# Performance work log

Measured on AMD Instinct MI355X. Metric: run time of the kernel, lower is better.

Reference implementation:

```python
import jax, jax.numpy as jnp
import numpy as np

N, E, G = 50000, 1250000, 256
IN, H, OUT = 64, 64, 2


def _glorot(k, shape):
    fan = shape[0] + shape[1]
    return jax.random.normal(k, shape, jnp.float32) * np.float32(np.sqrt(2.0 / fan))


def setup_inputs() -> dict:
    key = jax.random.key(0)
    ks = jax.random.split(key, 24)
    inp = {
        "x": jax.random.normal(ks[0], (N, IN), jnp.float32),
        "edge_index": jax.random.randint(ks[1], (2, E), 0, N, dtype=jnp.int32),
        "edge_weight": jax.random.uniform(ks[2], (E,), jnp.float32),
        "batch": jnp.sort(jax.random.randint(ks[3], (N,), 0, G, dtype=jnp.int32)),
    }
    # TransformerConv layer 1 (in=IN -> out=H, heads=1, edge_dim=1)
    inp["Wq1"] = _glorot(ks[4], (IN, H)); inp["bq1"] = jnp.zeros((H,), jnp.float32)
    inp["Wk1"] = _glorot(ks[5], (IN, H)); inp["bk1"] = jnp.zeros((H,), jnp.float32)
    inp["Wv1"] = _glorot(ks[6], (IN, H)); inp["bv1"] = jnp.zeros((H,), jnp.float32)
    inp["We1"] = _glorot(ks[7], (1, H))
    inp["Ws1"] = _glorot(ks[8], (IN, H)); inp["bs1"] = jnp.zeros((H,), jnp.float32)
    # TransformerConv layer 2 (H -> H)
    inp["Wq2"] = _glorot(ks[9], (H, H)); inp["bq2"] = jnp.zeros((H,), jnp.float32)
    inp["Wk2"] = _glorot(ks[10], (H, H)); inp["bk2"] = jnp.zeros((H,), jnp.float32)
    inp["Wv2"] = _glorot(ks[11], (H, H)); inp["bv2"] = jnp.zeros((H,), jnp.float32)
    inp["We2"] = _glorot(ks[12], (1, H))
    inp["Ws2"] = _glorot(ks[13], (H, H)); inp["bs2"] = jnp.zeros((H,), jnp.float32)
    # final linear
    inp["Wl"] = _glorot(ks[14], (H, OUT)); inp["bl"] = jnp.zeros((OUT,), jnp.float32)
    return inp


def _tconv(x, src, dst, e_attr, Wq, bq, Wk, bk, Wv, bv, We, Ws, bs, n):
    # PyG TransformerConv, heads=1, concat=True, root_weight=True, beta=False.
    d = Wq.shape[1]
    q = (x @ Wq + bq)[dst]            # [E, d] gather at target nodes
    k = (x @ Wk + bk)[src]            # [E, d] gather at source nodes
    v = (x @ Wv + bv)[src]            # [E, d]
    e = e_attr @ We                   # [E, d] edge embedding (no bias in PyG)
    alpha = jnp.sum(q * (k + e), axis=-1) / jnp.sqrt(jnp.float32(d))  # [E]
    # segment softmax over incoming edges of each target node
    amax = jax.ops.segment_max(alpha, dst, num_segments=n)
    amax = jnp.where(jnp.isfinite(amax), amax, jnp.float32(0.0))
    ex = jnp.exp(alpha - amax[dst])
    denom = jax.ops.segment_sum(ex, dst, num_segments=n)
    w = ex / jnp.maximum(denom[dst], jnp.float32(1e-16))
    out = jax.ops.segment_sum(w[:, None] * (v + e), dst, num_segments=n)  # [n, d]
    return out + x @ Ws + bs          # skip connection (lin_skip)


def reference(x, edge_index, edge_weight, batch,
              Wq1, bq1, Wk1, bk1, Wv1, bv1, We1, Ws1, bs1,
              Wq2, bq2, Wk2, bk2, Wv2, bv2, We2, Ws2, bs2,
              Wl, bl):
    src, dst = edge_index[0], edge_index[1]
    ea = edge_weight[:, None]  # edge_weight.unsqueeze(-1), edge_dim=1
    n = x.shape[0]
    h = jax.nn.relu(_tconv(x, src, dst, ea, Wq1, bq1, Wk1, bk1, Wv1, bv1, We1, Ws1, bs1, n))
    h = jax.nn.relu(_tconv(h, src, dst, ea, Wq2, bq2, Wk2, bk2, Wv2, bv2, We2, Ws2, bs2, n))
    # global_mean_pool over batch ids
    cnt = jax.ops.segment_sum(jnp.ones((n,), jnp.float32), batch, num_segments=G)
    pooled = jax.ops.segment_sum(h, batch, num_segments=G) / jnp.maximum(cnt, 1.0)[:, None]
    return pooled @ Wl + bl
```

## Files before the change

### kernel.cpp

```cpp
#include <hip/hip_runtime.h>
#include <hip/hip_fp16.h>

#define NN 50000
#define NE 1250000
#define NE4 312500
#define NG 256
#define NBKT 782
#define BCAP 2048
#define TILE 4096
#define NTB 306

#define QSCALE 0.18033688011112042f
#define EXP2 __builtin_amdgcn_exp2f

#if defined(__has_builtin)
#  if __has_builtin(__builtin_amdgcn_fdot2)
#    define HAS_FDOT2 1
#  endif
#endif

typedef _Float16 h2vec __attribute__((ext_vector_type(2)));

static __device__ __forceinline__ float fdot2f(unsigned a, unsigned b, float c) {
#ifdef HAS_FDOT2
    return __builtin_amdgcn_fdot2(__builtin_bit_cast(h2vec, a),
                                  __builtin_bit_cast(h2vec, b), c, false);
#else
    float2 fa = __half22float2(__builtin_bit_cast(__half2, a));
    float2 fb = __half22float2(__builtin_bit_cast(__half2, b));
    return fmaf(fa.x, fb.x, fmaf(fa.y, fb.y, c));
#endif
}

static __device__ __forceinline__ unsigned h2u(__half2 h) {
    return __builtin_bit_cast(unsigned, h);
}

__global__ void k_zero(int* __restrict__ gCursor) {
    int i = blockIdx.x * 256 + threadIdx.x;
    if (i < NBKT) gCursor[i] = 0;
}

__global__ void k_bscatter(const int* __restrict__ src, const int* __restrict__ dst,
                           const float* __restrict__ ew, int* __restrict__ gCursor,
                           unsigned* __restrict__ bbuf) {
    __shared__ int cnt[NBKT];
    __shared__ int base[NBKT];
    for (int i = threadIdx.x; i < NBKT; i += 256) cnt[i] = 0;
    __syncthreads();
    const int4* s4 = (const int4*)src;
    const int4* d4 = (const int4*)dst;
    const float4* w4 = (const float4*)ew;
    int b4 = blockIdx.x * (TILE / 4);
    unsigned rec[16]; int bkt[16];
    #pragma unroll
    for (int j = 0; j < 4; j++) {
        int i4 = b4 + j * 256 + threadIdx.x;
        if (i4 < NE4) {
            int4 s = s4[i4]; int4 d = d4[i4]; float4 w = w4[i4];
            int b0 = d.x >> 6, b1 = d.y >> 6, b2 = d.z >> 6, b3 = d.w >> 6;
            bkt[4*j+0] = b0; bkt[4*j+1] = b1; bkt[4*j+2] = b2; bkt[4*j+3] = b3;
            rec[4*j+0] = (unsigned)s.x | ((unsigned)(d.x & 63) << 16) | ((unsigned)(w.x * 1023.f + 0.5f) << 22);
            rec[4*j+1] = (unsigned)s.y | ((unsigned)(d.y & 63) << 16) | ((unsigned)(w.y * 1023.f + 0.5f) << 22);
            rec[4*j+2] = (unsigned)s.z | ((unsigned)(d.z & 63) << 16) | ((unsigned)(w.z * 1023.f + 0.5f) << 22);
            rec[4*j+3] = (unsigned)s.w | ((unsigned)(d.w & 63) << 16) | ((unsigned)(w.w * 1023.f + 0.5f) << 22);
            atomicAdd(&cnt[b0], 1); atomicAdd(&cnt[b1], 1);
            atomicAdd(&cnt[b2], 1); atomicAdd(&cnt[b3], 1);
        } else {
            bkt[4*j+0] = -1; bkt[4*j+1] = -1; bkt[4*j+2] = -1; bkt[4*j+3] = -1;
        }
    }
    __syncthreads();
    for (int i = threadIdx.x; i < NBKT; i += 256)
        base[i] = cnt[i] ? (i << 11) + atomicAdd(&gCursor[i], cnt[i]) : 0;
    __syncthreads();
    #pragma unroll
    for (int j = 0; j < 16; j++) {
        if (bkt[j] >= 0) {
            int pos = atomicAdd(&base[bkt[j]], 1);
            if (pos < ((bkt[j] + 1) << 11)) bbuf[pos] = rec[j];
        }
    }
}

__global__ void k_bsort(const int* __restrict__ gCursor, const unsigned* __restrict__ bbuf,
                        int* __restrict__ off, int* __restrict__ deg,
                        unsigned* __restrict__ pairP) {
    int b = blockIdx.x;
    int st = b << 11;
    int ce = gCursor[b]; if (ce > BCAP) ce = BCAP;
    __shared__ unsigned sbuf[BCAP];
    __shared__ int h[64];
    __shared__ int cur[64];
    if (threadIdx.x < 64) h[threadIdx.x] = 0;
    __syncthreads();
    for (int i = threadIdx.x; i < ce; i += 256) {
        unsigned r = bbuf[st + i];
        sbuf[i] = r;
        atomicAdd(&h[(r >> 16) & 63], 1);
    }
    __syncthreads();
    if (threadIdx.x < 64) {
        int v = h[threadIdx.x];
        int inc = v;
        #pragma unroll
        for (int o = 1; o < 64; o <<= 1) {
            int tmp = __shfl_up(inc, o);
            if (threadIdx.x >= o) inc += tmp;
        }
        int exc = st + inc - v;
        cur[threadIdx.x] = exc;
        int n = b * 64 + threadIdx.x;
        if (n < NN) { off[n] = exc; deg[n] = v; }
    }
    __syncthreads();
    for (int i = threadIdx.x; i < ce; i += 256) {
        unsigned r = sbuf[i];
        int pos = atomicAdd(&cur[(r >> 16) & 63], 1);
        float w = (float)(r >> 22) * (1.f / 1023.f);
        unsigned hw = (unsigned)__half_as_ushort(__float2half(w));
        pairP[pos] = (r & 0xFFFFu) | (hw << 16);
    }
}

__global__ __launch_bounds__(256, 4)
void k_linear(const float* __restrict__ xin,
              const float* __restrict__ Wq, const float* __restrict__ bq,
              const float* __restrict__ Wk, const float* __restrict__ bk,
              const float* __restrict__ Wv, const float* __restrict__ bv,
              const float* __restrict__ Ws, const float* __restrict__ bs,
              __half* __restrict__ qh, __half* __restrict__ kvh,
              float* __restrict__ agg) {
    int tid = threadIdx.x;
    int mat = tid >> 6, feat = tid & 63;
    const float* W = mat == 0 ? Wq : mat == 1 ? Wk : mat == 2 ? Wv : Ws;
    const float* b = mat == 0 ? bq : mat == 1 ? bk : mat == 2 ? bv : bs;

    float wcol[64];
    #pragma unroll
    for (int k = 0; k < 64; k++) wcol[k] = W[k * 64 + feat];
    float bias = b[feat];
    int kvoff = feat + (mat == 2 ? 64 : 0);

    __shared__ __align__(16) float sx[16 * 64];
    const float4* x4 = (const float4*)xin;

    int n0 = blockIdx.x * 16;
    if (n0 >= NN) return;
    float4 nxt = x4[n0 * 16 + tid];
    int stride = gridDim.x * 16;

    for (; n0 < NN; n0 += stride) {
        __syncthreads();
        ((float4*)sx)[tid] = nxt;
        __syncthreads();
        int n1 = n0 + stride;
        if (n1 < NN) nxt = x4[n1 * 16 + tid];
        for (int c = 0; c < 16; c++) {
            const float4* sxc = (const float4*)(sx + c * 64);
            float a0 = bias, a1 = 0.f, a2 = 0.f, a3 = 0.f;
            #pragma unroll
            for (int k4 = 0; k4 < 16; k4 += 4) {
                float4 v0 = sxc[k4 + 0], v1 = sxc[k4 + 1];
                float4 v2 = sxc[k4 + 2], v3 = sxc[k4 + 3];
                a0 = fmaf(v0.x, wcol[4 * k4 + 0], a0);
                a0 = fmaf(v0.y, wcol[4 * k4 + 1], a0);
                a0 = fmaf(v0.z, wcol[4 * k4 + 2], a0);
                a0 = fmaf(v0.w, wcol[4 * k4 + 3], a0);
                a1 = fmaf(v1.x, wcol[4 * k4 + 4], a1);
                a1 = fmaf(v1.y, wcol[4 * k4 + 5], a1);
                a1 = fmaf(v1.z, wcol[4 * k4 + 6], a1);
                a1 = fmaf(v1.w, wcol[4 * k4 + 7], a1);
                a2 = fmaf(v2.x, wcol[4 * k4 + 8], a2);
                a2 = fmaf(v2.y, wcol[4 * k4 + 9], a2);
                a2 = fmaf(v2.z, wcol[4 * k4 + 10], a2);
                a2 = fmaf(v2.w, wcol[4 * k4 + 11], a2);
                a3 = fmaf(v3.x, wcol[4 * k4 + 12], a3);
                a3 = fmaf(v3.y, wcol[4 * k4 + 13], a3);
                a3 = fmaf(v3.z, wcol[4 * k4 + 14], a3);
                a3 = fmaf(v3.w, wcol[4 * k4 + 15], a3);
            }
            float acc = (a0 + a1) + (a2 + a3);
            int nn = n0 + c;
            if (mat == 0)      qh[nn * 64 + feat] = __float2half(acc * QSCALE);
            else if (mat == 3) agg[nn * 64 + feat] = acc;
            else               kvh[nn * 128 + kvoff] = __float2half(acc);
        }
    }
}

__global__ void k_edge(const unsigned* __restrict__ pairP, const int* __restrict__ off,
                       const int* __restrict__ deg,
                       const __half* __restrict__ qh, const uint4* __restrict__ kv16,
                       const float* __restrict__ We, const float* __restrict__ aggin,
                       float* __restrict__ outp) {
    long gid = (long)blockIdx.x * 256 + threadIdx.x;
    int n = (int)(gid >> 6);
    if (n >= NN) return;
    int lane = threadIdx.x & 63;
    int g = lane >> 3, l = lane & 7;

    const uint4* q4 = (const uint4*)qh;
    uint4 qu = q4[n * 8 + l];
    const float4* wp = (const float4*)(We + l * 8);
    float4 wa = wp[0], wb = wp[1];
    unsigned we01 = h2u(__floats2half2_rn(wa.x, wa.y));
    unsigned we23 = h2u(__floats2half2_rn(wa.z, wa.w));
    unsigned we45 = h2u(__floats2half2_rn(wb.x, wb.y));
    unsigned we67 = h2u(__floats2half2_rn(wb.z, wb.w));

    int st = off[n], dg = deg[n];

    float qwe = fdot2f(qu.x, we01, fdot2f(qu.y, we23,
                fdot2f(qu.z, we45, fdot2f(qu.w, we67, 0.f))));
    qwe += __shfl_xor(qwe, 1); qwe += __shfl_xor(qwe, 2); qwe += __shfl_xor(qwe, 4);

    float den = 0.f, sw = 0.f;
    float acc[8] = {0.f, 0.f, 0.f, 0.f, 0.f, 0.f, 0.f, 0.f};

    auto edge = [&](unsigned pr, uint4 kk, uint4 vv) {
        float w = __half2float(__ushort_as_half((unsigned short)(pr >> 16)));
        float tA = fdot2f(qu.x, kk.x, fdot2f(qu.y, kk.y, 0.f));
        float tB = fdot2f(qu.z, kk.z, fdot2f(qu.w, kk.w, 0.f));
        float t = tA + tB;
        t += __shfl_xor(t, 1); t += __shfl_xor(t, 2); t += __shfl_xor(t, 4);
        t = fmaf(w, qwe, t);
        float p = EXP2(t);
        den += p;
        sw = fmaf(p, w, sw);
        float2 v0 = __half22float2(__builtin_bit_cast(__half2, vv.x));
        float2 v1 = __half22float2(__builtin_bit_cast(__half2, vv.y));
        float2 v2 = __half22float2(__builtin_bit_cast(__half2, vv.z));
        float2 v3 = __half22float2(__builtin_bit_cast(__half2, vv.w));
        acc[0] = fmaf(p, v0.x, acc[0]); acc[1] = fmaf(p, v0.y, acc[1]);
        acc[2] = fmaf(p, v1.x, acc[2]); acc[3] = fmaf(p, v1.y, acc[3]);
        acc[4] = fmaf(p, v2.x, acc[4]); acc[5] = fmaf(p, v2.y, acc[5]);
        acc[6] = fmaf(p, v3.x, acc[6]); acc[7] = fmaf(p, v3.y, acc[7]);
    };

    int nfull = dg >> 3;
    if (nfull > 0) {
        unsigned prA = pairP[st + g];
        unsigned prB = (nfull > 1) ? pairP[st + 8 + g] : 0u;
        unsigned rowA = prA & 0xFFFFu;
        uint4 kkA = kv16[rowA * 16 + l];
        uint4 vvA = kv16[rowA * 16 + 8 + l];
        for (int i = 0; i + 1 < nfull; i++) {
            unsigned prC = (i + 2 < nfull) ? pairP[st + (i + 2) * 8 + g] : 0u;
            unsigned rowB = prB & 0xFFFFu;
            uint4 kkB = kv16[rowB * 16 + l];
            uint4 vvB = kv16[rowB * 16 + 8 + l];
            edge(prA, kkA, vvA);
            prA = prB; kkA = kkB; vvA = vvB; prB = prC;
        }
        edge(prA, kkA, vvA);
    }
    int tl = nfull * 8 + g;
    if (tl < dg) {
        unsigned pr = pairP[st + tl];
        unsigned row = pr & 0xFFFFu;
        uint4 kk = kv16[row * 16 + l];
        uint4 vv = kv16[row * 16 + 8 + l];
        edge(pr, kk, vv);
    }

    #pragma unroll
    for (int o = 8; o <= 32; o <<= 1) {
        den += __shfl_xor(den, o);
        sw  += __shfl_xor(sw, o);
        #pragma unroll
        for (int j = 0; j < 8; j++) acc[j] += __shfl_xor(acc[j], o);
    }

    if (g == 0) {
        float inv = 1.f / fmaxf(den, 1e-16f);
        float swi = sw * inv;
        const float4* ain = (const float4*)(aggin + n * 64 + l * 8);
        float4 a0 = ain[0], a1 = ain[1];
        a0.x = fmaxf(fmaf(acc[0], inv, fmaf(swi, wa.x, a0.x)), 0.f);
        a0.y = fmaxf(fmaf(acc[1], inv, fmaf(swi, wa.y, a0.y)), 0.f);
        a0.z = fmaxf(fmaf(acc[2], inv, fmaf(swi, wa.z, a0.z)), 0.f);
        a0.w = fmaxf(fmaf(acc[3], inv, fmaf(swi, wa.w, a0.w)), 0.f);
        a1.x = fmaxf(fmaf(acc[4], inv, fmaf(swi, wb.x, a1.x)), 0.f);
        a1.y = fmaxf(fmaf(acc[5], inv, fmaf(swi, wb.y, a1.y)), 0.f);
        a1.z = fmaxf(fmaf(acc[6], inv, fmaf(swi, wb.z, a1.z)), 0.f);
        a1.w = fmaxf(fmaf(acc[7], inv, fmaf(swi, wb.w, a1.w)), 0.f);
        float4* ao = (float4*)(outp + n * 64 + l * 8);
        ao[0] = a0; ao[1] = a1;
    }
}

__global__ void k_final(const float* __restrict__ h, const int* __restrict__ batch,
                        const float* __restrict__ Wl, const float* __restrict__ bl,
                        float* __restrict__ out) {
    int g = blockIdx.x;
    int tid = threadIdx.x;
    int lo = 0, hi = NN;
    while (lo < hi) { int mid = (lo + hi) >> 1; if (batch[mid] < g) lo = mid + 1; else hi = mid; }
    int s0 = lo;
    hi = NN;
    while (lo < hi) { int mid = (lo + hi) >> 1; if (batch[mid] < g + 1) lo = mid + 1; else hi = mid; }
    int s1 = lo;

    int sub = tid >> 6, lane = tid & 63;
    float a = 0.f;
    for (int n = s0 + sub; n < s1; n += 4) a += h[n * 64 + lane];
    __shared__ float sred[4][64];
    sred[sub][lane] = a;
    __syncthreads();
    if (tid < 64) {
        float p = (sred[0][tid] + sred[1][tid] + sred[2][tid] + sred[3][tid])
                  / fmaxf((float)(s1 - s0), 1.f);
        float a0 = p * Wl[tid * 2 + 0];
        float a1 = p * Wl[tid * 2 + 1];
        #pragma unroll
        for (int o = 1; o < 64; o <<= 1) { a0 += __shfl_xor(a0, o); a1 += __shfl_xor(a1, o); }
        if (tid == 0) { out[g * 2 + 0] = a0 + bl[0]; out[g * 2 + 1] = a1 + bl[1]; }
    }
}

extern "C" void kernel_launch(void* const* d_in, const int* in_sizes, int n_in,
                              void* d_out, int out_size, void* d_ws, size_t ws_size,
                              hipStream_t stream) {
    const float* x    = (const float*)d_in[0];
    const int*   ei   = (const int*)d_in[1];
    const float* ew   = (const float*)d_in[2];
    const int*   batch= (const int*)d_in[3];
    const float *Wq1 = (const float*)d_in[4],  *bq1 = (const float*)d_in[5],
                *Wk1 = (const float*)d_in[6],  *bk1 = (const float*)d_in[7],
                *Wv1 = (const float*)d_in[8],  *bv1 = (const float*)d_in[9],
                *We1 = (const float*)d_in[10], *Ws1 = (const float*)d_in[11],
                *bs1 = (const float*)d_in[12],
                *Wq2 = (const float*)d_in[13], *bq2 = (const float*)d_in[14],
                *Wk2 = (const float*)d_in[15], *bk2 = (const float*)d_in[16],
                *Wv2 = (const float*)d_in[17], *bv2 = (const float*)d_in[18],
                *We2 = (const float*)d_in[19], *Ws2 = (const float*)d_in[20],
                *bs2 = (const float*)d_in[21],
                *Wl  = (const float*)d_in[22], *bl  = (const float*)d_in[23];
    const int* src = ei;
    const int* dst = ei + NE;
    float* out = (float*)d_out;

    float* p = (float*)d_ws;
    float* agg1 = p; p += (size_t)NN * 64;
    float* agg2 = p; p += (size_t)NN * 64;
    __half* qh  = (__half*)p; p += (size_t)NN * 32;
    __half* kvh = (__half*)p; p += (size_t)NN * 64;
    unsigned* bbuf  = (unsigned*)p; p += (size_t)NBKT * BCAP;
    unsigned* pairP = (unsigned*)p; p += (size_t)NBKT * BCAP;
    int* gCursor = (int*)p; p += NBKT;
    int* off     = (int*)p; p += NN;
    int* deg     = (int*)p; p += NN;

    dim3 b256(256);
    int wgrid = (int)(((long)NN * 64 + 255) / 256);

    k_zero<<<4, b256, 0, stream>>>(gCursor);
    k_bscatter<<<NTB, b256, 0, stream>>>(src, dst, ew, gCursor, bbuf);
    k_bsort<<<NBKT, b256, 0, stream>>>(gCursor, bbuf, off, deg, pairP);

    k_linear<<<1024, b256, 0, stream>>>(x, Wq1, bq1, Wk1, bk1, Wv1, bv1, Ws1, bs1,
                                        qh, kvh, agg1);
    k_edge<<<wgrid, b256, 0, stream>>>(pairP, off, deg, qh, (const uint4*)kvh, We1,
                                       agg1, agg1);

    k_linear<<<1024, b256, 0, stream>>>(agg1, Wq2, bq2, Wk2, bk2, Wv2, bv2, Ws2, bs2,
                                        qh, kvh, agg2);
    k_edge<<<wgrid, b256, 0, stream>>>(pairP, off, deg, qh, (const uint4*)kvh, We2,
                                       agg2, agg2);

    k_final<<<NG, b256, 0, stream>>>(agg2, batch, Wl, bl, out);
}
```

Baseline: 207.8 us.

## Stage bucket scatter and per-node sort in LDS for coalesced global writes

Measured after the change: 219.6 us. 5.7% more time.

```diff
diff --git a/kernel.cpp b/kernel.cpp
--- a/kernel.cpp
+++ b/kernel.cpp
@@ -45,7 +45,11 @@
                            const float* __restrict__ ew, int* __restrict__ gCursor,
                            unsigned* __restrict__ bbuf) {
     __shared__ int cnt[NBKT];
-    __shared__ int base[NBKT];
+    __shared__ int gbase[NBKT];
+    __shared__ int spos[NBKT];
+    __shared__ int sscan[256];
+    __shared__ unsigned staged[TILE];
+    __shared__ unsigned short sbkt[TILE];
     for (int i = threadIdx.x; i < NBKT; i += 256) cnt[i] = 0;
     __syncthreads();
     const int4* s4 = (const int4*)src;
@@ -71,15 +75,47 @@
         }
     }
     __syncthreads();
-    for (int i = threadIdx.x; i < NBKT; i += 256)
-        base[i] = cnt[i] ? (i << 11) + atomicAdd(&gCursor[i], cnt[i]) : 0;
+    int t = threadIdx.x;
+    int c[4]; int sum = 0;
+    #pragma unroll
+    for (int j = 0; j < 4; j++) {
+        int b = t * 4 + j;
+        c[j] = (b < NBKT) ? cnt[b] : 0;
+        sum += c[j];
+    }
+    sscan[t] = sum;
+    __syncthreads();
+    for (int o = 1; o < 256; o <<= 1) {
+        int tmp = (t >= o) ? sscan[t - o] : 0;
+        __syncthreads();
+        sscan[t] += tmp;
+        __syncthreads();
+    }
+    int run = sscan[t] - sum;
+    #pragma unroll
+    for (int j = 0; j < 4; j++) {
+        int b = t * 4 + j;
+        if (b < NBKT) {
+            spos[b] = run;
+            if (c[j]) gbase[b] = (b << 11) + atomicAdd(&gCursor[b], c[j]);
+            run += c[j];
+        }
+    }
     __syncthreads();
     #pragma unroll
     for (int j = 0; j < 16; j++) {
         if (bkt[j] >= 0) {
-            int pos = atomicAdd(&base[bkt[j]], 1);
-            if (pos < ((bkt[j] + 1) << 11)) bbuf[pos] = rec[j];
-        }
+            int p = atomicAdd(&spos[bkt[j]], 1);
+            staged[p] = rec[j];
+            sbkt[p] = (unsigned short)bkt[j];
+        }
+    }
+    __syncthreads();
+    int total = sscan[255];
+    for (int i = threadIdx.x; i < total; i += 256) {
+        int b = sbkt[i];
+        int gdest = gbase[b] + (i - (spos[b] - cnt[b]));
+        if (gdest < ((b + 1) << 11)) bbuf[gdest] = staged[i];
     }
 }
 
@@ -90,6 +126,7 @@
     int st = b << 11;
     int ce = gCursor[b]; if (ce > BCAP) ce = BCAP;
     __shared__ unsigned sbuf[BCAP];
+    __shared__ unsigned sout[BCAP];
     __shared__ int h[64];
     __shared__ int cur[64];
     if (threadIdx.x < 64) h[threadIdx.x] = 0;
@@ -108,10 +145,10 @@
             int tmp = __shfl_up(inc, o);
             if (threadIdx.x >= o) inc += tmp;
         }
-        int exc = st + inc - v;
+        int exc = inc - v;
         cur[threadIdx.x] = exc;
         int n = b * 64 + threadIdx.x;
-        if (n < NN) { off[n] = exc; deg[n] = v; }
+        if (n < NN) { off[n] = st + exc; deg[n] = v; }
     }
     __syncthreads();
     for (int i = threadIdx.x; i < ce; i += 256) {
@@ -119,8 +156,10 @@
         int pos = atomicAdd(&cur[(r >> 16) & 63], 1);
         float w = (float)(r >> 22) * (1.f / 1023.f);
         unsigned hw = (unsigned)__half_as_ushort(__float2half(w));
-        pairP[pos] = (r & 0xFFFFu) | (hw << 16);
-    }
+        sout[pos] = (r & 0xFFFFu) | (hw << 16);
+    }
+    __syncthreads();
+    for (int i = threadIdx.x; i < ce; i += 256) pairP[st + i] = sout[i];
 }
 
 __global__ __launch_bounds__(256, 4)
```

## Use coarser 256-node dst buckets and stage sorted edges in LDS

Applied to the files above, without the earlier changes.

Result: no change. 209.0 us (+0.6%).

```diff
diff --git a/kernel.cpp b/kernel.cpp
--- a/kernel.cpp
+++ b/kernel.cpp
@@ -5,8 +5,9 @@
 #define NE 1250000
 #define NE4 312500
 #define NG 256
-#define NBKT 782
-#define BCAP 2048
+#define NBKT 196
+#define BSH 13
+#define BCAP 8192
 #define TILE 4096
 #define NTB 306
 
@@ -37,7 +38,7 @@
 }
 
 __global__ void k_zero(int* __restrict__ gCursor) {
-    int i = blockIdx.x * 256 + threadIdx.x;
+    int i = threadIdx.x;
     if (i < NBKT) gCursor[i] = 0;
 }
 
@@ -46,7 +47,7 @@
                            unsigned* __restrict__ bbuf) {
     __shared__ int cnt[NBKT];
     __shared__ int base[NBKT];
-    for (int i = threadIdx.x; i < NBKT; i += 256) cnt[i] = 0;
+    if (threadIdx.x < NBKT) cnt[threadIdx.x] = 0;
     __syncthreads();
     const int4* s4 = (const int4*)src;
     const int4* d4 = (const int4*)dst;
@@ -58,12 +59,12 @@
         int i4 = b4 + j * 256 + threadIdx.x;
         if (i4 < NE4) {
             int4 s = s4[i4]; int4 d = d4[i4]; float4 w = w4[i4];
-            int b0 = d.x >> 6, b1 = d.y >> 6, b2 = d.z >> 6, b3 = d.w >> 6;
+            int b0 = d.x >> 8, b1 = d.y >> 8, b2 = d.z >> 8, b3 = d.w >> 8;
             bkt[4*j+0] = b0; bkt[4*j+1] = b1; bkt[4*j+2] = b2; bkt[4*j+3] = b3;
-            rec[4*j+0] = (unsigned)s.x | ((unsigned)(d.x & 63) << 16) | ((unsigned)(w.x * 1023.f + 0.5f) << 22);
-            rec[4*j+1] = (unsigned)s.y | ((unsigned)(d.y & 63) << 16) | ((unsigned)(w.y * 1023.f + 0.5f) << 22);
-            rec[4*j+2] = (unsigned)s.z | ((unsigned)(d.z & 63) << 16) | ((unsigned)(w.z * 1023.f + 0.5f) << 22);
-            rec[4*j+3] = (unsigned)s.w | ((unsigned)(d.w & 63) << 16) | ((unsigned)(w.w * 1023.f + 0.5f) << 22);
+            rec[4*j+0] = (unsigned)s.x | ((unsigned)(d.x & 255) << 16) | ((unsigned)(w.x * 255.f + 0.5f) << 24);
+            rec[4*j+1] = (unsigned)s.y | ((unsigned)(d.y & 255) << 16) | ((unsigned)(w.y * 255.f + 0.5f) << 24);
+            rec[4*j+2] = (unsigned)s.z | ((unsigned)(d.z & 255) << 16) | ((unsigned)(w.z * 255.f + 0.5f) << 24);
+            rec[4*j+3] = (unsigned)s.w | ((unsigned)(d.w & 255) << 16) | ((unsigned)(w.w * 255.f + 0.5f) << 24);
             atomicAdd(&cnt[b0], 1); atomicAdd(&cnt[b1], 1);
             atomicAdd(&cnt[b2], 1); atomicAdd(&cnt[b3], 1);
         } else {
@@ -71,14 +72,16 @@
         }
     }
     __syncthreads();
-    for (int i = threadIdx.x; i < NBKT; i += 256)
-        base[i] = cnt[i] ? (i << 11) + atomicAdd(&gCursor[i], cnt[i]) : 0;
+    if (threadIdx.x < NBKT) {
+        int c = cnt[threadIdx.x];
+        base[threadIdx.x] = c ? (threadIdx.x << BSH) + atomicAdd(&gCursor[threadIdx.x], c) : 0;
+    }
     __syncthreads();
     #pragma unroll
     for (int j = 0; j < 16; j++) {
         if (bkt[j] >= 0) {
             int pos = atomicAdd(&base[bkt[j]], 1);
-            if (pos < ((bkt[j] + 1) << 11)) bbuf[pos] = rec[j];
+            if (pos < ((bkt[j] + 1) << BSH)) bbuf[pos] = rec[j];
         }
     }
 }
@@ -87,40 +90,45 @@
                         int* __restrict__ off, int* __restrict__ deg,
                         unsigned* __restrict__ pairP) {
     int b = blockIdx.x;
-    int st = b << 11;
+    int st = b << BSH;
     int ce = gCursor[b]; if (ce > BCAP) ce = BCAP;
     __shared__ unsigned sbuf[BCAP];
-    __shared__ int h[64];
-    __shared__ int cur[64];
-    if (threadIdx.x < 64) h[threadIdx.x] = 0;
-    __syncthreads();
-    for (int i = threadIdx.x; i < ce; i += 256) {
+    __shared__ unsigned sout[BCAP];
+    __shared__ int h[256];
+    __shared__ int cur[256];
+    __shared__ int sscan[256];
+    int t = threadIdx.x;
+    h[t] = 0;
+    __syncthreads();
+    for (int i = t; i < ce; i += 256) {
         unsigned r = bbuf[st + i];
         sbuf[i] = r;
-        atomicAdd(&h[(r >> 16) & 63], 1);
-    }
-    __syncthreads();
-    if (threadIdx.x < 64) {
-        int v = h[threadIdx.x];
-        int inc = v;
-        #pragma unroll
-        for (int o = 1; o < 64; o <<= 1) {
-            int tmp = __shfl_up(inc, o);
-            if (threadIdx.x >= o) inc += tmp;
-        }
-        int exc = st + inc - v;
-        cur[threadIdx.x] = exc;
-        int n = b * 64 + threadIdx.x;
-        if (n < NN) { off[n] = exc; deg[n] = v; }
-    }
-    __syncthreads();
-    for (int i = threadIdx.x; i < ce; i += 256) {
+        atomicAdd(&h[(r >> 16) & 255], 1);
+    }
+    __syncthreads();
+    int v = h[t];
+    sscan[t] = v;
+    __syncthreads();
+    for (int o = 1; o < 256; o <<= 1) {
+        int tmp = (t >= o) ? sscan[t - o] : 0;
+        __syncthreads();
+        sscan[t] += tmp;
+        __syncthreads();
+    }
+    int exc = sscan[t] - v;
+    cur[t] = exc;
+    int n = b * 256 + t;
+    if (n < NN) { off[n] = st + exc; deg[n] = v; }
+    __syncthreads();
+    for (int i = t; i < ce; i += 256) {
         unsigned r = sbuf[i];
-        int pos = atomicAdd(&cur[(r >> 16) & 63], 1);
-        float w = (float)(r >> 22) * (1.f / 1023.f);
+        int pos = atomicAdd(&cur[(r >> 16) & 255], 1);
+        float w = (float)(r >> 24) * (1.f / 255.f);
         unsigned hw = (unsigned)__half_as_ushort(__float2half(w));
-        pairP[pos] = (r & 0xFFFFu) | (hw << 16);
-    }
+        sout[pos] = (r & 0xFFFFu) | (hw << 16);
+    }
+    __syncthreads();
+    for (int i = t; i < ce; i += 256) pairP[st + i] = sout[i];
 }
 
 __global__ __launch_bounds__(256, 4)
@@ -355,7 +363,7 @@
     dim3 b256(256);
     int wgrid = (int)(((long)NN * 64 + 255) / 256);
 
-    k_zero<<<4, b256, 0, stream>>>(gCursor);
+    k_zero<<<1, b256, 0, stream>>>(gCursor);
     k_bscatter<<<NTB, b256, 0, stream>>>(src, dst, ew, gCursor, bbuf);
     k_bsort<<<NBKT, b256, 0, stream>>>(gCursor, bbuf, off, deg, pairP);
 
```
